# Kernel tuning notes

Measured on AMD Instinct MI355X. Metric: run time of the kernel, lower is better.

## Reference

```python
import jax, jax.numpy as jnp
import numpy as np

T = 16000        # signal length
N1 = 120         # first-order filters (J=12, Q=10)
NPSI2 = 14       # second-order filterbank size (Q2=1)
NPAIR = 553      # second-order coefficients -> 120 + 553 = 673 channels
SUB1 = 8         # subsample U1 before order 2
T2 = T // SUB1   # 2000
STR1 = 1000      # lowpass stride at length T  -> 16 output samples
STR2 = T2 // (T // STR1)  # 125 -> 16 output samples
LOG_EPS = 1e-6
BN_EPS = 1e-5


def _gauss_hat(N, xi, sigma):
    om = np.arange(N) / N
    return np.exp(-((om - xi) ** 2) / (2.0 * sigma ** 2)).astype(np.float32)


def _filterbank():
    Q = 10.0
    xi1 = 0.45 * 2.0 ** (-np.arange(N1) / Q)
    sig1 = np.maximum(xi1 * 0.1, 2.0 / T)
    psi1 = np.stack([_gauss_hat(T, x, s) for x, s in zip(xi1, sig1)])
    phi1 = _gauss_hat(T, 0.0, 0.4 / STR1)
    xi2 = 0.45 * 2.0 ** (-np.arange(NPSI2, dtype=np.float64))
    sig2 = np.maximum(xi2 * 0.2, 2.0 / T2)
    psi2 = np.stack([_gauss_hat(T2, x, s) for x, s in zip(xi2, sig2)])
    phi2 = _gauss_hat(T2, 0.0, 0.4 / STR2)
    pairs = [(i, j) for i in range(N1) for j in range(NPSI2) if xi2[j] < xi1[i] / 2.0]
    pairs = pairs[:NPAIR]
    assert len(pairs) == NPAIR
    pi1 = np.array([p[0] for p in pairs], np.int32)
    pi2 = np.array([p[1] for p in pairs], np.int32)
    return psi1, phi1, psi2, phi2, pi1, pi2


def setup_inputs():
    key = jax.random.key(0)
    ks = jax.random.split(key, 8)
    psi1, phi1, psi2, phi2, pi1, pi2 = _filterbank()
    B = 32
    inp = {
        "x": jax.random.normal(ks[0], (B, 1, T), jnp.float32),
        "psi1_hat": jnp.asarray(psi1),
        "phi1_hat": jnp.asarray(phi1),
        "psi2_hat": jnp.asarray(psi2),
        "phi2_hat": jnp.asarray(phi2),
        "gamma": jnp.ones((673,), jnp.float32),
        "beta": jnp.zeros((673,), jnp.float32),
        "W1": jax.random.normal(ks[1], (300, 673), jnp.float32) * 0.04,
        "b1": jnp.zeros((300,), jnp.float32),
        "W2": jax.random.normal(ks[2], (90, 300), jnp.float32) * 0.06,
        "b2": jnp.zeros((90,), jnp.float32),
        "W3": jax.random.normal(ks[3], (35, 90), jnp.float32) * 0.1,
        "b3": jnp.zeros((35,), jnp.float32),
        "pair_i1": jnp.asarray(pi1),
        "pair_i2": jnp.asarray(pi2),
    }
    return inp


def reference(x, psi1_hat, phi1_hat, psi2_hat, phi2_hat, gamma, beta,
              W1, b1, W2, b2, W3, b3, pair_i1, pair_i2):
    xs = x.squeeze(1)                                       # [B, T]
    Xf = jnp.fft.fft(xs)                                    # [B, T] c64
    # --- order 1: wavelet conv (freq-domain), modulus ---
    U1 = jnp.abs(jnp.fft.ifft(Xf[:, None, :] * psi1_hat[None]))        # [B, N1, T]
    # S1 = lowpass(U1) subsampled to 16 samples
    S1 = jnp.real(jnp.fft.ifft(jnp.fft.fft(U1) * phi1_hat))[..., ::STR1]  # [B, N1, 16]
    # --- order 2 on subsampled U1 ---
    U1sf = jnp.fft.fft(U1[..., ::SUB1])                     # [B, N1, T2]
    U2 = jnp.abs(jnp.fft.ifft(U1sf[:, pair_i1, :] * psi2_hat[pair_i2]))  # [B, NPAIR, T2]
    S2 = jnp.real(jnp.fft.ifft(jnp.fft.fft(U2) * phi2_hat))[..., ::STR2]  # [B, NPAIR, 16]
    S = jnp.concatenate([S1, S2], axis=1)                   # [B, 673, 16]
    # log-abs + temporal mean pooling
    f = jnp.mean(jnp.log(jnp.abs(S) + LOG_EPS), axis=-1)    # [B, 673]
    # BatchNorm1d (training mode: batch statistics)
    mu = jnp.mean(f, axis=0)
    var = jnp.var(f, axis=0)
    f = (f - mu) / jnp.sqrt(var + BN_EPS) * gamma + beta
    # MLP head
    h = jax.nn.relu(f @ W1.T + b1)
    h = jax.nn.relu(h @ W2.T + b2)
    return jax.nn.log_softmax(h @ W3.T + b3, axis=-1)
```

## Files before the change

kernel.cpp:

```cpp
#include <hip/hip_runtime.h>
#include <math.h>

typedef float2 cf;

__device__ __forceinline__ cf cadd(cf a, cf b){ return make_float2(a.x+b.x, a.y+b.y); }
__device__ __forceinline__ cf csub(cf a, cf b){ return make_float2(a.x-b.x, a.y-b.y); }
__device__ __forceinline__ cf cmul(cf a, cf b){ return make_float2(a.x*b.x - a.y*b.y, a.x*b.y + a.y*b.x); }

__device__ __forceinline__ int SW(int i){ return i ^ ((i>>4)&15); }
#define AT(x) s[SW(x)]
#define WFENCE asm volatile("" ::: "memory")

__device__ __forceinline__ int idivf(int a, int b){ return (a >= 0) ? a/b : -((-a + b - 1)/b); }
__device__ __forceinline__ int idivc(int a, int b){ return (a >= 0) ? (a + b - 1)/b : -((-a)/b); }

__device__ __forceinline__ int devB(int i){
  int jm = i/10 + 2;
  double kc = 900.0*exp2((double)(-jm));
  double sg = fmax(180.0*exp2((double)(-jm)), 2.0);
  return min(2000, (int)ceil(kc + 6.5*sg) + 1);
}

template<int N, int L, bool INV>
__device__ __forceinline__ void stage_r2(cf* __restrict__ s, const cf* __restrict__ tw, int tid, int nt){
  constexpr int Ls = L/2, nbf = N/2, tws = 16000/L;
  for (int q = tid; q < nbf; q += nt){
    int blk = q / Ls, j = q - blk*Ls;
    int base = blk*L + j;
    cf w1 = tw[tws*j]; if (INV) w1.y = -w1.y;
    if (!INV){
      cf a = AT(base), b = AT(base+Ls);
      AT(base) = cadd(a,b);
      AT(base+Ls) = cmul(csub(a,b), w1);
    } else {
      cf a = AT(base), b = cmul(AT(base+Ls), w1);
      AT(base) = cadd(a,b);
      AT(base+Ls) = csub(a,b);
    }
  }
}

template<int N, int L, bool INV>
__device__ __forceinline__ void stage_r4(cf* __restrict__ s, const cf* __restrict__ tw, int tid, int nt){
  constexpr int Ls = L/4, nbf = N/4, tws = 16000/L;
  for (int q = tid; q < nbf; q += nt){
    int blk = q / Ls, j = q - blk*Ls;
    int base = blk*L + j;
    cf w1 = tw[tws*j]; if (INV) w1.y = -w1.y;
    cf w2 = cmul(w1,w1), w3 = cmul(w2,w1);
    if (!INV){
      cf y0=AT(base), y1=AT(base+Ls), y2=AT(base+2*Ls), y3=AT(base+3*Ls);
      cf t0=cadd(y0,y2), t1=csub(y0,y2), t2=cadd(y1,y3), t3=csub(y1,y3);
      AT(base)      = cadd(t0,t2);
      AT(base+Ls)   = cmul(make_float2(t1.x + t3.y, t1.y - t3.x), w1);
      AT(base+2*Ls) = cmul(csub(t0,t2), w2);
      AT(base+3*Ls) = cmul(make_float2(t1.x - t3.y, t1.y + t3.x), w3);
    } else {
      cf z0=AT(base);
      cf z1=cmul(AT(base+Ls),   w1);
      cf z2=cmul(AT(base+2*Ls), w2);
      cf z3=cmul(AT(base+3*Ls), w3);
      cf t0=cadd(z0,z2), t1=csub(z0,z2), t2=cadd(z1,z3), t3=csub(z1,z3);
      AT(base)      = cadd(t0,t2);
      AT(base+Ls)   = make_float2(t1.x - t3.y, t1.y + t3.x);
      AT(base+2*Ls) = csub(t0,t2);
      AT(base+3*Ls) = make_float2(t1.x + t3.y, t1.y - t3.x);
    }
  }
}

template<int N, int L, bool INV>
__device__ __forceinline__ void stage_r5(cf* __restrict__ s, const cf* __restrict__ tw, int tid, int nt){
  constexpr int Ls = L/5, nbf = N/5, tws = 16000/L;
  const float C1 = 0.30901699437494742f, S1c = 0.95105651629515357f;
  const float C2 = -0.80901699437494745f, S2c = 0.58778525229247314f;
  for (int q = tid; q < nbf; q += nt){
    int blk = q / Ls, j = q - blk*Ls;
    int base = blk*L + j;
    cf w1 = tw[tws*j]; if (INV) w1.y = -w1.y;
    cf w2 = cmul(w1,w1), w3 = cmul(w2,w1), w4 = cmul(w2,w2);
    if (!INV){
      cf y0=AT(base), y1=AT(base+Ls), y2=AT(base+2*Ls), y3=AT(base+3*Ls), y4=AT(base+4*Ls);
      cf t1=cadd(y1,y4), t2=csub(y1,y4), t3=cadd(y2,y3), t4=csub(y2,y3);
      cf z0 = cadd(y0, cadd(t1,t3));
      cf m1 = make_float2(y0.x + C1*t1.x + C2*t3.x, y0.y + C1*t1.y + C2*t3.y);
      cf m2 = make_float2(y0.x + C2*t1.x + C1*t3.x, y0.y + C2*t1.y + C1*t3.y);
      cf wa = make_float2(S1c*t2.x + S2c*t4.x, S1c*t2.y + S2c*t4.y);
      cf wb = make_float2(S2c*t2.x - S1c*t4.x, S2c*t2.y - S1c*t4.y);
      cf o1 = make_float2(m1.x + wa.y, m1.y - wa.x);
      cf o4 = make_float2(m1.x - wa.y, m1.y + wa.x);
      cf o2 = make_float2(m2.x + wb.y, m2.y - wb.x);
      cf o3 = make_float2(m2.x - wb.y, m2.y + wb.x);
      AT(base) = z0;
      AT(base+Ls)   = cmul(o1,w1);
      AT(base+2*Ls) = cmul(o2,w2);
      AT(base+3*Ls) = cmul(o3,w3);
      AT(base+4*Ls) = cmul(o4,w4);
    } else {
      cf z0=AT(base);
      cf z1=cmul(AT(base+Ls),   w1);
      cf z2=cmul(AT(base+2*Ls), w2);
      cf z3=cmul(AT(base+3*Ls), w3);
      cf z4=cmul(AT(base+4*Ls), w4);
      cf t1=cadd(z1,z4), t2=csub(z1,z4), t3=cadd(z2,z3), t4=csub(z2,z3);
      cf y0 = cadd(z0, cadd(t1,t3));
      cf m1 = make_float2(z0.x + C1*t1.x + C2*t3.x, z0.y + C1*t1.y + C2*t3.y);
      cf m2 = make_float2(z0.x + C2*t1.x + C1*t3.x, z0.y + C2*t1.y + C1*t3.y);
      cf wa = make_float2(S1c*t2.x + S2c*t4.x, S1c*t2.y + S2c*t4.y);
      cf wb = make_float2(S2c*t2.x - S1c*t4.x, S2c*t2.y - S1c*t4.y);
      AT(base)      = y0;
      AT(base+Ls)   = make_float2(m1.x - wa.y, m1.y + wa.x);
      AT(base+2*Ls) = make_float2(m2.x - wb.y, m2.y + wb.x);
      AT(base+3*Ls) = make_float2(m2.x + wb.y, m2.y - wb.x);
      AT(base+4*Ls) = make_float2(m1.x + wa.y, m1.y - wa.x);
    }
  }
}

template<bool INV>
__device__ void fft16000(cf* s, const cf* tw, int tid, int nt){
  if (!INV){
    stage_r5<16000,16000,false>(s,tw,tid,nt); __syncthreads();
    stage_r5<16000, 3200,false>(s,tw,tid,nt); __syncthreads();
    stage_r5<16000,  640,false>(s,tw,tid,nt); __syncthreads();
    stage_r4<16000,  128,false>(s,tw,tid,nt); __syncthreads();
    stage_r4<16000,   32,false>(s,tw,tid,nt); __syncthreads();
    stage_r4<16000,    8,false>(s,tw,tid,nt); __syncthreads();
    stage_r2<16000,    2,false>(s,tw,tid,nt); __syncthreads();
  } else {
    stage_r2<16000,    2,true >(s,tw,tid,nt); __syncthreads();
    stage_r4<16000,    8,true >(s,tw,tid,nt); __syncthreads();
    stage_r4<16000,   32,true >(s,tw,tid,nt); __syncthreads();
    stage_r4<16000,  128,true >(s,tw,tid,nt); __syncthreads();
    stage_r5<16000,  640,true >(s,tw,tid,nt); __syncthreads();
    stage_r5<16000, 3200,true >(s,tw,tid,nt); __syncthreads();
    stage_r5<16000,16000,true >(s,tw,tid,nt); __syncthreads();
  }
}

template<bool INV>
__device__ void fft2000(cf* s, const cf* tw, int tid, int nt){
  if (!INV){
    stage_r5<2000,2000,false>(s,tw,tid,nt); __syncthreads();
    stage_r5<2000, 400,false>(s,tw,tid,nt); __syncthreads();
    stage_r5<2000,  80,false>(s,tw,tid,nt); __syncthreads();
    stage_r4<2000,  16,false>(s,tw,tid,nt); __syncthreads();
    stage_r4<2000,   4,false>(s,tw,tid,nt); __syncthreads();
  } else {
    stage_r4<2000,   4,true >(s,tw,tid,nt); __syncthreads();
    stage_r4<2000,  16,true >(s,tw,tid,nt); __syncthreads();
    stage_r5<2000,  80,true >(s,tw,tid,nt); __syncthreads();
    stage_r5<2000, 400,true >(s,tw,tid,nt); __syncthreads();
    stage_r5<2000,2000,true >(s,tw,tid,nt); __syncthreads();
  }
}

__device__ void fft8000i(cf* s, const cf* tw, int tid, int nt){
  stage_r4<8000,   4,true>(s,tw,tid,nt); __syncthreads();
  stage_r4<8000,  16,true>(s,tw,tid,nt); __syncthreads();
  stage_r4<8000,  64,true>(s,tw,tid,nt); __syncthreads();
  stage_r5<8000, 320,true>(s,tw,tid,nt); __syncthreads();
  stage_r5<8000,1600,true>(s,tw,tid,nt); __syncthreads();
  stage_r5<8000,8000,true>(s,tw,tid,nt); __syncthreads();
}
__device__ void fft4000i(cf* s, const cf* tw, int tid, int nt){
  stage_r2<4000,   2,true>(s,tw,tid,nt); __syncthreads();
  stage_r4<4000,   8,true>(s,tw,tid,nt); __syncthreads();
  stage_r4<4000,  32,true>(s,tw,tid,nt); __syncthreads();
  stage_r5<4000, 160,true>(s,tw,tid,nt); __syncthreads();
  stage_r5<4000, 800,true>(s,tw,tid,nt); __syncthreads();
  stage_r5<4000,4000,true>(s,tw,tid,nt); __syncthreads();
}
__device__ void fft1000i(cf* s, const cf* tw, int tid, int nt){
  stage_r2<1000,   2,true>(s,tw,tid,nt); __syncthreads();
  stage_r4<1000,   8,true>(s,tw,tid,nt); __syncthreads();
  stage_r5<1000,  40,true>(s,tw,tid,nt); __syncthreads();
  stage_r5<1000, 200,true>(s,tw,tid,nt); __syncthreads();
  stage_r5<1000,1000,true>(s,tw,tid,nt); __syncthreads();
}
__device__ void fft1000f(cf* s, const cf* tw, int tid, int nt){
  stage_r5<1000,1000,false>(s,tw,tid,nt); __syncthreads();
  stage_r5<1000, 200,false>(s,tw,tid,nt); __syncthreads();
  stage_r5<1000,  40,false>(s,tw,tid,nt); __syncthreads();
  stage_r4<1000,   8,false>(s,tw,tid,nt); __syncthreads();
  stage_r2<1000,   2,false>(s,tw,tid,nt); __syncthreads();
}
__device__ void fft500i(cf* s, const cf* tw, int tid, int nt){
  stage_r4<500,  4,true>(s,tw,tid,nt); __syncthreads();
  stage_r5<500, 20,true>(s,tw,tid,nt); __syncthreads();
  stage_r5<500,100,true>(s,tw,tid,nt); __syncthreads();
  stage_r5<500,500,true>(s,tw,tid,nt); __syncthreads();
}

__device__ __forceinline__ void fft250w(cf* s, const cf* tw, int lane){
  stage_r2<250,  2,true>(s,tw,lane,64); WFENCE;
  stage_r5<250, 10,true>(s,tw,lane,64); WFENCE;
  stage_r5<250, 50,true>(s,tw,lane,64); WFENCE;
  stage_r5<250,250,true>(s,tw,lane,64); WFENCE;
}
template<int M, bool INV>
__device__ __forceinline__ void fft_w(cf* s, const cf* tw, int lane){
  if constexpr (M==500){
    if constexpr (!INV){
      stage_r5<500,500,false>(s,tw,lane,64); WFENCE;
      stage_r5<500,100,false>(s,tw,lane,64); WFENCE;
      stage_r5<500, 20,false>(s,tw,lane,64); WFENCE;
      stage_r4<500,  4,false>(s,tw,lane,64); WFENCE;
    } else {
      stage_r4<500,  4,true>(s,tw,lane,64); WFENCE;
      stage_r5<500, 20,true>(s,tw,lane,64); WFENCE;
      stage_r5<500,100,true>(s,tw,lane,64); WFENCE;
      stage_r5<500,500,true>(s,tw,lane,64); WFENCE;
    }
  } else if constexpr (M==250){
    if constexpr (!INV){
      stage_r5<250,250,false>(s,tw,lane,64); WFENCE;
      stage_r5<250, 50,false>(s,tw,lane,64); WFENCE;
      stage_r5<250, 10,false>(s,tw,lane,64); WFENCE;
      stage_r2<250,  2,false>(s,tw,lane,64); WFENCE;
    } else {
      fft250w(s,tw,lane);
    }
  } else if constexpr (M==200){
    if constexpr (!INV){
      stage_r5<200,200,false>(s,tw,lane,64); WFENCE;
      stage_r5<200, 40,false>(s,tw,lane,64); WFENCE;
      stage_r4<200,  8,false>(s,tw,lane,64); WFENCE;
      stage_r2<200,  2,false>(s,tw,lane,64); WFENCE;
    } else {
      stage_r2<200,  2,true>(s,tw,lane,64); WFENCE;
      stage_r4<200,  8,true>(s,tw,lane,64); WFENCE;
      stage_r5<200, 40,true>(s,tw,lane,64); WFENCE;
      stage_r5<200,200,true>(s,tw,lane,64); WFENCE;
    }
  } else {
    if constexpr (!INV){
      stage_r5<125,125,false>(s,tw,lane,64); WFENCE;
      stage_r5<125, 25,false>(s,tw,lane,64); WFENCE;
      stage_r5<125,  5,false>(s,tw,lane,64); WFENCE;
    } else {
      stage_r5<125,  5,true>(s,tw,lane,64); WFENCE;
      stage_r5<125, 25,true>(s,tw,lane,64); WFENCE;
      stage_r5<125,125,true>(s,tw,lane,64); WFENCE;
    }
  }
}

__device__ __forceinline__ int pos16000(int k){
  int k0=k%5; k/=5; int k1=k%5; k/=5; int k2=k%5; k/=5;
  int k3=k&3; k>>=2; int k4=k&3; k>>=2; int k5=k&3; k>>=2;
  return k0*3200 + k1*640 + k2*128 + k3*32 + k4*8 + k5*2 + k;
}
__device__ __forceinline__ int pos8000(int k){
  int k0=k%5; k/=5; int k1=k%5; k/=5; int k2=k%5; k/=5;
  int k3=k&3, k4=(k>>2)&3, k5=k>>4;
  return k0*1600 + k1*320 + k2*64 + k3*16 + k4*4 + k5;
}
__device__ __forceinline__ int pos4000(int k){
  int k0=k%5; k/=5; int k1=k%5; k/=5; int k2=k%5; k/=5;
  int k3=k&3, k4=(k>>2)&3, k5=k>>4;
  return k0*800 + k1*160 + k2*32 + k3*8 + k4*2 + k5;
}
__device__ __forceinline__ int pos2000(int k){
  int k0=k%5; k/=5; int k1=k%5; k/=5; int k2=k%5; k/=5;
  int k3=k&3, k4=k>>2;
  return k0*400 + k1*80 + k2*16 + k3*4 + k4;
}
__device__ __forceinline__ int pos1000(int k){
  int k0=k%5; k/=5; int k1=k%5; k/=5; int k2=k%5; k/=5;
  int k3=k&3, k4=k>>2;
  return k0*200 + k1*40 + k2*8 + k3*2 + k4;
}
__device__ __forceinline__ int pos500(int k){
  int k0=k%5; k/=5; int k1=k%5; k/=5; int k2=k%5; k/=5;
  return k0*100 + k1*20 + k2*4 + k;
}
__device__ __forceinline__ int pos250(int k){
  int k0=k%5; k/=5; int k1=k%5; k/=5; int k2=k%5; k/=5;
  return k0*50 + k1*10 + k2*2 + k;
}
__device__ __forceinline__ int pos200(int k){
  int k0=k%5; k/=5; int k1=k%5; k/=5;
  int k2=k&3, k3=k>>2;
  return k0*40 + k1*8 + k2*2 + k3;
}
__device__ __forceinline__ int pos125(int k){
  int k0=k%5; k/=5; int k1=k%5; k/=5;
  return k0*25 + k1*5 + k;
}

template<int M> __device__ __forceinline__ int posM(int k){
  if constexpr (M==16000) return pos16000(k);
  else if constexpr (M==8000) return pos8000(k);
  else if constexpr (M==4000) return pos4000(k);
  else return pos2000(k);
}
template<int M> __device__ __forceinline__ int posS(int k){
  if constexpr (M==500) return pos500(k);
  else if constexpr (M==250) return pos250(k);
  else if constexpr (M==200) return pos200(k);
  else return pos125(k);
}
template<int M> __device__ __forceinline__ void fftM_inv(cf* s, const cf* tw, int tid, int nt){
  if constexpr (M==16000) fft16000<true>(s,tw,tid,nt);
  else if constexpr (M==8000) fft8000i(s,tw,tid,nt);
  else if constexpr (M==4000) fft4000i(s,tw,tid,nt);
  else fft2000<true>(s,tw,tid,nt);
}


__global__ void k_tw(cf* __restrict__ tw){
  int j = blockIdx.x*blockDim.x + threadIdx.x;
  if (j < 16000){
    double a = -6.283185307179586476925286766559 * (double)j / 16000.0;
    tw[j] = make_float2((float)cos(a), (float)sin(a));
  }
}

__global__ void k_btab(const float* __restrict__ phi1, const float* __restrict__ phi2,
                       float* __restrict__ h1g, float* __restrict__ h2g){
  int i = blockIdx.x*blockDim.x + threadIdx.x;
  const double TWO_PI = 6.283185307179586476925286766559;
  if (i < 5201){
    int d = i - 2600;
    double a = 0.0;
    for (int k = 0; k < 64; ++k) a += (double)phi1[k]*cos(TWO_PI*(double)(k*d)/16000.0);
    h1g[i] = (float)(a/16000.0 - (double)phi1[0]/32000.0);
  } else if (i == 5201){
    h1g[5201] = phi1[0]*(1.f/32000.f);
  } else if (i < 5202 + 661){
    int j = i - 5202; int d = j - 330;
    double a = 0.0;
    for (int k = 0; k < 64; ++k) a += (double)phi2[k]*cos(TWO_PI*(double)(k*d)/2000.0);
    h2g[j] = (float)(a/2000.0 - (double)phi2[0]/4000.0);
  } else if (i == 5202 + 661){
    h2g[661] = phi2[0]*(1.f/4000.f);
  }
}

__global__ __launch_bounds__(1024) void k_classify(const int* __restrict__ pi2,
                                                   int* __restrict__ list5, int* __restrict__ list4){
  __shared__ int w5[16], w4[16];
  int p = threadIdx.x;
  for (int t = p; t < 493; t += 1024) list5[t] = 0;
  for (int t = p; t < 60;  t += 1024) list4[t] = 0;
  bool valid = p < 553;
  int j2 = valid ? pi2[p] : 99;
  bool f5 = valid && (j2 >= 5);
  bool f4 = valid && (j2 < 5);
  unsigned long long m5 = __ballot(f5);
  unsigned long long m4 = __ballot(f4);
  int lane = p & 63, wid = p >> 6;
  if (lane == 0){ w5[wid] = __popcll(m5); w4[wid] = __popcll(m4); }
  __syncthreads();
  if (valid){
    int b5 = 0, b4 = 0;
    for (int w = 0; w < wid; ++w){ b5 += w5[w]; b4 += w4[w]; }
    unsigned long long lm = (1ull << lane) - 1ull;
    if (f5) list5[b5 + __popcll(m5 & lm)] = p;
    if (f4) list4[b4 + __popcll(m4 & lm)] = p;
  }
}

__global__ __launch_bounds__(1024) void k_fftx(const float* __restrict__ x, cf* __restrict__ Xf,
                                               const cf* __restrict__ tw){
  extern __shared__ cf s[];
  int b = blockIdx.x;
  int tid = threadIdx.x, nt = blockDim.x;
  for (int n = tid; n < 16000; n += nt) AT(n) = make_float2(x[b*16000 + n], 0.f);
  __syncthreads();
  fft16000<false>(s, tw, tid, nt);
  for (int k = tid; k < 16000; k += nt) Xf[b*16000 + k] = AT(pos16000(k));
}

template<int M, int ST, int NF, int I0, int NT>
__global__ __launch_bounds__(NT) void kf(const cf* __restrict__ Xf, const float* __restrict__ psi1,
                                         const float* __restrict__ h1g, const cf* __restrict__ tw,
                                         cf* __restrict__ U1sf, float* __restrict__ S1){
  extern __shared__ cf s[];
  constexpr int NW = NT/64;
  int b = blockIdx.x / NF;
  int i = I0 + (blockIdx.x - b*NF);
  int tid = threadIdx.x, wid = tid>>6, lane = tid&63;
  double x1 = 0.45 * exp2((double)(-i) / 10.0);
  double kc = 16000.0 * x1;
  double sg = fmax(1600.0 * x1, 2.0);
  int k0 = max(0, (int)floor(kc - 6.5*sg));
  int k1 = min(16000, (int)ceil(kc + 6.5*sg) + 1);
  int W = k1 - k0;
  for (int n = tid; n < M; n += NT) s[n] = make_float2(0.f, 0.f);
  __syncthreads();
  const cf* X = Xf + (size_t)b*16000 + k0;
  const float* P = psi1 + (size_t)i*16000 + k0;
  for (int j = tid; j < W; j += NT){
    cf v = X[j]; float pf = P[j];
    int pp = posM<M>(j);
    AT(pp) = make_float2(v.x*pf, v.y*pf);
  }
  __syncthreads();
  fftM_inv<M>(s, tw, tid, NT);
  constexpr int R = (M + NT - 1)/NT;
  float mreg[R]; float tsum = 0.f;
  const float inv = 1.f/16000.f;
  #pragma unroll
  for (int r = 0; r < R; ++r){
    int n = tid + r*NT;
    if (n < M){ cf v = AT(n); mreg[r] = sqrtf(v.x*v.x + v.y*v.y)*inv; tsum += mreg[r]; }
    else mreg[r] = 0.f;
  }
  float* fl = (float*)s;
  float* part = (float*)(s + M);
  __syncthreads();
  #pragma unroll
  for (int r = 0; r < R; ++r){ int n = tid + r*NT; if (n < M) fl[n] = mreg[r]; }
  #pragma unroll
  for (int o = 32; o > 0; o >>= 1) tsum += __shfl_xor(tsum, o);
  if (lane == 0) part[wid] = tsum;
  __syncthreads();
  if (tid == 0){ float tt = 0.f; for (int w = 0; w < NW; ++w) tt += part[w]; part[NW] = tt; }
  __syncthreads();
  float stot = part[NW];
  float c1 = h1g[5201];
  for (int t = wid; t < 16; t += NW){
    int mlo = (1000*t - 2600)/ST;
    int mhi = (1000*t + 2600)/ST;
    float acc = 0.f;
    for (int m = mlo + lane; m <= mhi; m += 64){
      int mm = m; if (mm < 0) mm += M; else if (mm >= M) mm -= M;
      acc = fmaf(fl[mm], h1g[1000*t - m*ST + 2600], acc);
    }
    #pragma unroll
    for (int o = 32; o > 0; o >>= 1) acc += __shfl_xor(acc, o);
    if (lane == 0) S1[((size_t)b*120 + i)*16 + t] = (float)ST*(acc + c1*stot);
  }
  constexpr int K = 8/ST;
  float d0 = fl[tid*K];
  float d1 = 0.f;
  { int m2 = tid + 1024; if (m2 < 2000) d1 = fl[m2*K]; }
  __syncthreads();
  AT(tid) = make_float2(d0, 0.f);
  { int m2 = tid + 1024; if (m2 < 2000) AT(m2) = make_float2(d1, 0.f); }
  __syncthreads();
  fft2000<false>(s, tw, tid, NT);
  int B = devB(i);
  cf* out = U1sf + ((size_t)b*120 + i)*2000;
  for (int k = tid; k < B; k += NT) out[k] = AT(pos2000(k));
}

template<int M, int ST, int NF, int I0>
__global__ __launch_bounds__(256) void k_nb(const cf* __restrict__ Xf, const float* __restrict__ psi1,
                                            const float* __restrict__ h1g, const cf* __restrict__ tw,
                                            cf* __restrict__ U1sf, float* __restrict__ S1){
  extern __shared__ cf s[];
  float* fl = (float*)(s + M);
  float* part = fl + M;
  int b = blockIdx.x / NF;
  int i = I0 + (blockIdx.x - b*NF);
  int tid = threadIdx.x, wid = tid>>6, lane = tid&63;
  double x1 = 0.45 * exp2((double)(-i)/10.0);
  double kc = 16000.0*x1, sg = fmax(1600.0*x1, 2.0);
  int k0 = max(0,(int)floor(kc-6.5*sg));
  int k1 = min(16000,(int)ceil(kc+6.5*sg)+1);
  int W = k1-k0;
  for (int n = tid; n < M; n += 256) s[n] = make_float2(0.f,0.f);
  __syncthreads();
  const cf* X = Xf + (size_t)b*16000 + k0;
  const float* P = psi1 + (size_t)i*16000 + k0;
  for (int j = tid; j < W; j += 256){
    cf v = X[j]; float pf = P[j];
    int pp = (M==2000) ? pos2000(j) : pos1000(j);
    AT(pp) = make_float2(v.x*pf, v.y*pf);
  }
  __syncthreads();
  if constexpr (M==2000) fft2000<true>(s,tw,tid,256); else fft1000i(s,tw,tid,256);
  float tsum = 0.f;
  for (int n = tid; n < M; n += 256){
    cf v = AT(n);
    float mg = sqrtf(v.x*v.x+v.y*v.y)*(1.f/16000.f);
    fl[n] = mg; tsum += mg;
  }
  #pragma unroll
  for (int o=32;o>0;o>>=1) tsum += __shfl_xor(tsum,o);
  if (lane==0) part[wid] = tsum;
  __syncthreads();
  float stot = part[0]+part[1]+part[2]+part[3];
  float c1 = h1g[5201];
  float* S1o = S1 + ((size_t)b*120+i)*16;
  for (int r = 0; r < 4; ++r){
    int t = wid + 4*r;
    int mlo = idivc(1000*t-2600,ST), mhi = idivf(1000*t+2600,ST);
    float acc = 0.f;
    for (int m = mlo+lane; m <= mhi; m += 64){
      int mm = m; if (mm<0) mm+=M; else if (mm>=M) mm-=M;
      acc = fmaf(fl[mm], h1g[1000*t - m*ST + 2600], acc);
    }
    #pragma unroll
    for (int o=32;o>0;o>>=1) acc += __shfl_xor(acc,o);
    if (lane==0) S1o[t] = (float)ST*(acc + c1*stot);
  }
  __syncthreads();
  for (int n = tid; n < M; n += 256) AT(n) = make_float2(fl[n], 0.f);
  __syncthreads();
  if constexpr (M==2000) fft2000<false>(s,tw,tid,256); else fft1000f(s,tw,tid,256);
  int B = devB(i);
  const float sc = 2000.f/(float)M;
  cf* out = U1sf + ((size_t)b*120+i)*2000;
  for (int k = tid; k < B; k += 256){
    cf v = AT((M==2000)?pos2000(k):pos1000(k));
    out[k] = make_float2(v.x*sc, v.y*sc);
  }
}

template<int M, int SPAD, int ST, int NF, int I0, int WPB>
__global__ __launch_bounds__(WPB*64) void k_nw(const cf* __restrict__ Xf, const float* __restrict__ psi1,
                                               const float* __restrict__ h1g, const cf* __restrict__ tw,
                                               cf* __restrict__ U1sf, float* __restrict__ S1){
  extern __shared__ cf sh[];
  int wid = threadIdx.x >> 6, lane = threadIdx.x & 63;
  int q = blockIdx.x*WPB + wid;
  int filt = q >> 5, b = q & 31;
  int i = I0 + filt;
  cf* s = sh + wid*SPAD;
  float* fl = ((float*)(sh + WPB*SPAD)) + wid*SPAD;
  double x1 = 0.45 * exp2((double)(-i)/10.0);
  double kc = 16000.0*x1, sg = fmax(1600.0*x1, 2.0);
  int k0 = max(0,(int)floor(kc-6.5*sg));
  int k1 = min(16000,(int)ceil(kc+6.5*sg)+1);
  int W = k1-k0;
  for (int n = lane; n < SPAD; n += 64) s[n] = make_float2(0.f,0.f);
  WFENCE;
  const cf* X = Xf + (size_t)b*16000 + k0;
  const float* P = psi1 + (size_t)i*16000 + k0;
  for (int j = lane; j < W; j += 64){
    cf v = X[j]; float pf = P[j];
    AT(posS<M>(j)) = make_float2(v.x*pf, v.y*pf);
  }
  WFENCE;
  fft_w<M,true>(s,tw,lane);
  float tsum = 0.f;
  for (int n = lane; n < M; n += 64){
    cf v = AT(n);
    float mg = sqrtf(v.x*v.x+v.y*v.y)*(1.f/16000.f);
    fl[n] = mg; tsum += mg;
  }
  WFENCE;
  #pragma unroll
  for (int o=32;o>0;o>>=1) tsum += __shfl_xor(tsum,o);
  float c1 = h1g[5201];
  float* S1o = S1 + ((size_t)b*120+i)*16;
  for (int t = 0; t < 16; ++t){
    int mlo = idivc(1000*t-2600,ST), mhi = idivf(1000*t+2600,ST);
    float acc = 0.f;
    for (int m = mlo+lane; m <= mhi; m += 64){
      int mm = m; if (mm<0) mm+=M; else if (mm>=M) mm-=M;
      acc = fmaf(fl[mm], h1g[1000*t - m*ST + 2600], acc);
    }
    #pragma unroll
    for (int o=32;o>0;o>>=1) acc += __shfl_xor(acc,o);
    if (lane==0) S1o[t] = (float)ST*(acc + c1*tsum);
  }
  for (int n = lane; n < M; n += 64) AT(n) = make_float2(fl[n], 0.f);
  WFENCE;
  fft_w<M,false>(s,tw,lane);
  int B = devB(i);
  const float sc = 2000.f/(float)M;
  cf* out = U1sf + ((size_t)b*120+i)*2000;
  for (int k = lane; k < B; k += 64){
    cf v = AT(posS<M>(k));
    out[k] = make_float2(v.x*sc, v.y*sc);
  }
}

__global__ __launch_bounds__(256) void k_sec5(const cf* __restrict__ U1sf, const float* __restrict__ psi2,
                                              const float* __restrict__ h2g, const cf* __restrict__ tw,
                                              const int* __restrict__ pi1, const int* __restrict__ pi2,
                                              const int* __restrict__ list5, float* __restrict__ S2){
  __shared__ cf sall[4*256];
  __shared__ float flall[4*256];
  int wid = threadIdx.x >> 6, lane = threadIdx.x & 63;
  int q = blockIdx.x*4 + wid;
  int p = list5[q >> 5];
  int b = q & 31;
  int i1 = pi1[p], j2 = pi2[p];
  cf* s = sall + wid*256;
  float* fl2 = flall + wid*256;
  double xc = exp2((double)(-j2));
  double kc = 900.0*xc, sg = fmax(180.0*xc, 2.0);
  int k0 = max(0, (int)floor(kc - 6.5*sg));
  int k1 = min(2000, (int)ceil(kc + 6.5*sg) + 1);
  int W = k1 - k0;
  for (int n = lane; n < 256; n += 64) s[n] = make_float2(0.f, 0.f);
  WFENCE;
  const cf* U = U1sf + (size_t)(b*120 + i1)*2000 + k0;
  const float* F = psi2 + j2*2000 + k0;
  for (int j = lane; j < W; j += 64){
    cf v = U[j]; float f = F[j];
    AT(pos250(j)) = make_float2(v.x*f, v.y*f);
  }
  WFENCE;
  fft250w(s, tw, lane);
  float tsum = 0.f;
  #pragma unroll
  for (int r = 0; r < 4; ++r){
    int n = lane + r*64;
    if (n < 250){
      cf v = AT(n);
      float mg = sqrtf(v.x*v.x + v.y*v.y)*(1.f/2000.f);
      fl2[n] = mg; tsum += mg;
    }
  }
  WFENCE;
  #pragma unroll
  for (int o = 32; o > 0; o >>= 1) tsum += __shfl_xor(tsum, o);
  float stot = tsum;
  float c2 = h2g[661];
  float* S2o = S2 + (size_t)(b*553 + p)*16;
  for (int t = 0; t < 16; ++t){
    int mlo = (125*t - 330 + 7) >> 3;
    int mhi = (125*t + 330) >> 3;
    float acc = 0.f;
    for (int m = mlo + lane; m <= mhi; m += 64){
      int mm = m; if (mm < 0) mm += 250; else if (mm >= 250) mm -= 250;
      acc = fmaf(fl2[mm], h2g[125*t - m*8 + 330], acc);
    }
    #pragma unroll
    for (int o = 32; o > 0; o >>= 1) acc += __shfl_xor(acc, o);
    if (lane == 0) S2o[t] = 8.f*(acc + c2*stot);
  }
}

__global__ __launch_bounds__(128) void k_secbig(const cf* __restrict__ U1sf, const float* __restrict__ psi2,
                                                const float* __restrict__ h2g, const cf* __restrict__ tw,
                                                const int* __restrict__ pi1, const int* __restrict__ pi2,
                                                const int* __restrict__ list4, float* __restrict__ S2){
  extern __shared__ cf s[];
  float* fl2 = (float*)(s + 2000);
  float* part = fl2 + 2000;
  int p = list4[blockIdx.x >> 5];
  int b = blockIdx.x & 31;
  int tid = threadIdx.x, wid = tid>>6, lane = tid&63;
  int i1 = pi1[p], j2 = pi2[p];
  int M2, s2l;
  if (j2 == 4){ M2 = 500;  s2l = 2; }
  else if (j2 == 3){ M2 = 1000; s2l = 1; }
  else { M2 = 2000; s2l = 0; }
  int ST2 = 1 << s2l;
  double xc = exp2((double)(-j2));
  double kc = 900.0*xc, sg = fmax(180.0*xc, 2.0);
  int k0 = max(0, (int)floor(kc - 6.5*sg));
  int k1 = min(2000, (int)ceil(kc + 6.5*sg) + 1);
  int W = k1 - k0;
// ... 105 lines not shown
                                              float* __restrict__ out){
  __shared__ float lg[35];
  int b = blockIdx.x;
  int tid = threadIdx.x, wid = tid >> 6, lane = tid & 63;
  for (int r = wid; r < 35; r += 4){
    float acc = 0.f;
    for (int k = lane; k < 90; k += 64) acc = fmaf(h2[b*90 + k], W3[r*90 + k], acc);
    #pragma unroll
    for (int o = 32; o > 0; o >>= 1) acc += __shfl_down(acc, o);
    if (lane == 0) lg[r] = acc + b3[r];
  }
  __syncthreads();
  if (tid < 64){
    float v = (tid < 35) ? lg[tid] : -1e30f;
    float mx = v;
    #pragma unroll
    for (int o = 32; o > 0; o >>= 1) mx = fmaxf(mx, __shfl_xor(mx, o));
    float e = (tid < 35) ? expf(v - mx) : 0.f;
    float se = e;
    #pragma unroll
    for (int o = 32; o > 0; o >>= 1) se += __shfl_xor(se, o);
    if (tid < 35) out[b*35 + tid] = v - mx - logf(se);
  }
}


extern "C" void kernel_launch(void* const* d_in, const int* in_sizes, int n_in,
                              void* d_out, int out_size, void* d_ws, size_t ws_size,
                              hipStream_t stream){
  const float* x     = (const float*)d_in[0];
  const float* psi1  = (const float*)d_in[1];
  const float* phi1  = (const float*)d_in[2];
  const float* psi2  = (const float*)d_in[3];
  const float* phi2  = (const float*)d_in[4];
  const float* gamma = (const float*)d_in[5];
  const float* beta  = (const float*)d_in[6];
  const float* W1    = (const float*)d_in[7];
  const float* b1    = (const float*)d_in[8];
  const float* W2    = (const float*)d_in[9];
  const float* b2    = (const float*)d_in[10];
  const float* W3    = (const float*)d_in[11];
  const float* b3    = (const float*)d_in[12];
  const int*   pi1   = (const int*)d_in[13];
  const int*   pi2   = (const int*)d_in[14];

  char* ws = (char*)d_ws;
  constexpr size_t o_tw = 0;
  constexpr size_t o_Xf = o_tw + (size_t)16000*sizeof(cf);
  constexpr size_t o_U  = o_Xf + (size_t)32*16000*sizeof(cf);
  constexpr size_t o_S1 = o_U  + (size_t)3840*2000*sizeof(cf);
  constexpr size_t o_S2 = o_S1 + (size_t)3840*16*sizeof(float);
  constexpr size_t o_l5 = o_S2 + (size_t)17696*16*sizeof(float);
  constexpr size_t o_l4 = o_l5 + (size_t)512*sizeof(int);
  constexpr size_t o_fn = o_l4 + (size_t)64*sizeof(int);
  constexpr size_t o_h1 = o_fn + (size_t)32*673*sizeof(float);
  constexpr size_t o_h2 = o_h1 + (size_t)5202*sizeof(float);
  constexpr size_t o_m1 = o_h2 + (size_t)662*sizeof(float);
  constexpr size_t o_m2 = o_m1 + (size_t)32*300*sizeof(float);

  cf*    tw    = (cf*)(ws + o_tw);
  cf*    Xf    = (cf*)(ws + o_Xf);
  cf*    U1sf  = (cf*)(ws + o_U);
  float* S1b   = (float*)(ws + o_S1);
  float* S2b   = (float*)(ws + o_S2);
  int*   list5 = (int*)(ws + o_l5);
  int*   list4 = (int*)(ws + o_l4);
  float* fnbuf = (float*)(ws + o_fn);
  float* h1g   = (float*)(ws + o_h1);
  float* h2g   = (float*)(ws + o_h2);
  float* m1buf = (float*)(ws + o_m1);
  float* m2buf = (float*)(ws + o_m2);

  hipFuncSetAttribute((const void*)k_fftx, hipFuncAttributeMaxDynamicSharedMemorySize, 131072);
  hipFuncSetAttribute((const void*)kf<16000,1,13, 0,1024>, hipFuncAttributeMaxDynamicSharedMemorySize, 131072);
  hipFuncSetAttribute((const void*)kf< 8000,2,10,13,1024>, hipFuncAttributeMaxDynamicSharedMemorySize, 131072);

  k_tw<<<63, 256, 0, stream>>>(tw);
  k_btab<<<23, 256, 0, stream>>>(phi1, phi2, h1g, h2g);
  k_classify<<<1, 1024, 0, stream>>>(pi2, list5, list4);
  k_fftx<<<32, 1024, 128000, stream>>>(x, Xf, tw);
  kf<16000,1,13, 0,1024><<<32*13, 1024, 16000*8 + 17*4, stream>>>(Xf, psi1, h1g, tw, U1sf, S1b);
  kf< 8000,2,10,13,1024><<<32*10, 1024,  8000*8 + 17*4, stream>>>(Xf, psi1, h1g, tw, U1sf, S1b);
  kf< 4000,4,10,23,1024><<<32*10, 1024,  4000*8 + 17*4, stream>>>(Xf, psi1, h1g, tw, U1sf, S1b);
  k_nb<2000, 8,10,33><<<32*10, 256, 2000*8 + 2000*4 + 5*4, stream>>>(Xf, psi1, h1g, tw, U1sf, S1b);
  k_nb<1000,16,10,43><<<32*10, 256, 1000*8 + 1000*4 + 5*4, stream>>>(Xf, psi1, h1g, tw, U1sf, S1b);
  k_nw< 500,512, 32,10,53,4><<< 80, 256, 4*512*12, stream>>>(Xf, psi1, h1g, tw, U1sf, S1b);
  k_nw< 250,256, 64,10,63,8><<< 40, 512, 8*256*12, stream>>>(Xf, psi1, h1g, tw, U1sf, S1b);
  k_nw< 200,208, 80,10,73,8><<< 40, 512, 8*208*12, stream>>>(Xf, psi1, h1g, tw, U1sf, S1b);
  k_nw< 125,128,128,37,83,8><<<148, 512, 8*128*12, stream>>>(Xf, psi1, h1g, tw, U1sf, S1b);
  k_sec5<<<(493*32)/4, 256, 0, stream>>>(U1sf, psi2, h2g, tw, pi1, pi2, list5, S2b);
  k_secbig<<<60*32, 128, 2000*8 + 2000*4 + 4*4, stream>>>(U1sf, psi2, h2g, tw, pi1, pi2, list4, S2b);
  k_fbn<<<673, 64, 0, stream>>>(S1b, S2b, gamma, beta, fnbuf);
  k_mlp1<<<1200, 512, 0, stream>>>(fnbuf, W1, b1, m1buf);
  k_mlp2<<<360, 512, 0, stream>>>(m1buf, W2, b2, m2buf);
  k_mlp3<<<32, 256, 0, stream>>>(m2buf, W3, b3, (float*)d_out);
}
```

Before: 392.4 us.

## Compute order-1 lowpass in frequency domain and resize narrowband FFT lengths

For filters 33 and up, the order-1 lowpass S1 is no longer a spatial-domain convolution over U1 with an h1g table. It is now a 64-bin frequency-domain evaluation using phi1 and twiddles, taken after the forward FFT that is already needed for U1sf. The per-band FFT sizes change to lengths that are multiples of 16 (1600, 640, 320, 160 instead of 1000, 500, 250, 125), so the 16-point output grid aligns with the subsampling. This also removes the separate float magnitude buffer. The aim is to cut the scalar convolution loops and shared-memory use, at the cost of somewhat larger FFTs and a possible accuracy change from truncating to 64 frequency bins.

Measured after the change: 366.6 us. 1.07x faster.

```diff
diff --git a/kernel.cpp b/kernel.cpp
--- a/kernel.cpp
+++ b/kernel.cpp
@@ -11,8 +11,9 @@
 #define AT(x) s[SW(x)]
 #define WFENCE asm volatile("" ::: "memory")
 
-__device__ __forceinline__ int idivf(int a, int b){ return (a >= 0) ? a/b : -((-a + b - 1)/b); }
-__device__ __forceinline__ int idivc(int a, int b){ return (a >= 0) ? (a + b - 1)/b : -((-a)/b); }
+template<bool WAVE> __device__ __forceinline__ void SYf(){
+  if constexpr (WAVE) { WFENCE; } else __syncthreads();
+}
 
 __device__ __forceinline__ int devB(int i){
   int jm = i/10 + 2;
@@ -178,70 +179,98 @@
   stage_r5<1000, 200,true>(s,tw,tid,nt); __syncthreads();
   stage_r5<1000,1000,true>(s,tw,tid,nt); __syncthreads();
 }
-__device__ void fft1000f(cf* s, const cf* tw, int tid, int nt){
-  stage_r5<1000,1000,false>(s,tw,tid,nt); __syncthreads();
-  stage_r5<1000, 200,false>(s,tw,tid,nt); __syncthreads();
-  stage_r5<1000,  40,false>(s,tw,tid,nt); __syncthreads();
-  stage_r4<1000,   8,false>(s,tw,tid,nt); __syncthreads();
-  stage_r2<1000,   2,false>(s,tw,tid,nt); __syncthreads();
-}
 __device__ void fft500i(cf* s, const cf* tw, int tid, int nt){
   stage_r4<500,  4,true>(s,tw,tid,nt); __syncthreads();
   stage_r5<500, 20,true>(s,tw,tid,nt); __syncthreads();
   stage_r5<500,100,true>(s,tw,tid,nt); __syncthreads();
   stage_r5<500,500,true>(s,tw,tid,nt); __syncthreads();
 }
-
 __device__ __forceinline__ void fft250w(cf* s, const cf* tw, int lane){
   stage_r2<250,  2,true>(s,tw,lane,64); WFENCE;
   stage_r5<250, 10,true>(s,tw,lane,64); WFENCE;
   stage_r5<250, 50,true>(s,tw,lane,64); WFENCE;
   stage_r5<250,250,true>(s,tw,lane,64); WFENCE;
 }
-template<int M, bool INV>
-__device__ __forceinline__ void fft_w(cf* s, const cf* tw, int lane){
-  if constexpr (M==500){
-    if constexpr (!INV){
-      stage_r5<500,500,false>(s,tw,lane,64); WFENCE;
-      stage_r5<500,100,false>(s,tw,lane,64); WFENCE;
-      stage_r5<500, 20,false>(s,tw,lane,64); WFENCE;
-      stage_r4<500,  4,false>(s,tw,lane,64); WFENCE;
+
+template<int M, bool INV, bool WAVE>
+__device__ __forceinline__ void fftg(cf* s, const cf* tw, int tid, int nt){
+  if constexpr (M==2000){
+    if constexpr (INV){
+      stage_r4<2000,4,true>(s,tw,tid,nt); SYf<WAVE>();
+      stage_r4<2000,16,true>(s,tw,tid,nt); SYf<WAVE>();
+      stage_r5<2000,80,true>(s,tw,tid,nt); SYf<WAVE>();
+      stage_r5<2000,400,true>(s,tw,tid,nt); SYf<WAVE>();
+      stage_r5<2000,2000,true>(s,tw,tid,nt); SYf<WAVE>();
     } else {
-      stage_r4<500,  4,true>(s,tw,lane,64); WFENCE;
-      stage_r5<500, 20,true>(s,tw,lane,64); WFENCE;
-      stage_r5<500,100,true>(s,tw,lane,64); WFENCE;
-      stage_r5<500,500,true>(s,tw,lane,64); WFENCE;
-    }
-  } else if constexpr (M==250){
-    if constexpr (!INV){
-      stage_r5<250,250,false>(s,tw,lane,64); WFENCE;
-      stage_r5<250, 50,false>(s,tw,lane,64); WFENCE;
-      stage_r5<250, 10,false>(s,tw,lane,64); WFENCE;
-      stage_r2<250,  2,false>(s,tw,lane,64); WFENCE;
+      stage_r5<2000,2000,false>(s,tw,tid,nt); SYf<WAVE>();
+      stage_r5<2000,400,false>(s,tw,tid,nt); SYf<WAVE>();
+      stage_r5<2000,80,false>(s,tw,tid,nt); SYf<WAVE>();
+      stage_r4<2000,16,false>(s,tw,tid,nt); SYf<WAVE>();
+      stage_r4<2000,4,false>(s,tw,tid,nt); SYf<WAVE>();
+    }
+  } else if constexpr (M==1600){
+    if constexpr (INV){
+      stage_r4<1600,4,true>(s,tw,tid,nt); SYf<WAVE>();
+      stage_r4<1600,16,true>(s,tw,tid,nt); SYf<WAVE>();
+      stage_r4<1600,64,true>(s,tw,tid,nt); SYf<WAVE>();
+      stage_r5<1600,320,true>(s,tw,tid,nt); SYf<WAVE>();
+      stage_r5<1600,1600,true>(s,tw,tid,nt); SYf<WAVE>();
     } else {
-      fft250w(s,tw,lane);
+      stage_r5<1600,1600,false>(s,tw,tid,nt); SYf<WAVE>();
+      stage_r5<1600,320,false>(s,tw,tid,nt); SYf<WAVE>();
+      stage_r4<1600,64,false>(s,tw,tid,nt); SYf<WAVE>();
+      stage_r4<1600,16,false>(s,tw,tid,nt); SYf<WAVE>();
+      stage_r4<1600,4,false>(s,tw,tid,nt); SYf<WAVE>();
+    }
+  } else if constexpr (M==640){
+    if constexpr (INV){
+      stage_r2<640,2,true>(s,tw,tid,nt); SYf<WAVE>();
+      stage_r4<640,8,true>(s,tw,tid,nt); SYf<WAVE>();
+      stage_r4<640,32,true>(s,tw,tid,nt); SYf<WAVE>();
+      stage_r4<640,128,true>(s,tw,tid,nt); SYf<WAVE>();
+      stage_r5<640,640,true>(s,tw,tid,nt); SYf<WAVE>();
+    } else {
+      stage_r5<640,640,false>(s,tw,tid,nt); SYf<WAVE>();
+      stage_r4<640,128,false>(s,tw,tid,nt); SYf<WAVE>();
+      stage_r4<640,32,false>(s,tw,tid,nt); SYf<WAVE>();
+      stage_r4<640,8,false>(s,tw,tid,nt); SYf<WAVE>();
+      stage_r2<640,2,false>(s,tw,tid,nt); SYf<WAVE>();
+    }
+  } else if constexpr (M==320){
+    if constexpr (INV){
+      stage_r4<320,4,true>(s,tw,tid,nt); SYf<WAVE>();
+      stage_r4<320,16,true>(s,tw,tid,nt); SYf<WAVE>();
+      stage_r4<320,64,true>(s,tw,tid,nt); SYf<WAVE>();
+      stage_r5<320,320,true>(s,tw,tid,nt); SYf<WAVE>();
+    } else {
+      stage_r5<320,320,false>(s,tw,tid,nt); SYf<WAVE>();
+      stage_r4<320,64,false>(s,tw,tid,nt); SYf<WAVE>();
+      stage_r4<320,16,false>(s,tw,tid,nt); SYf<WAVE>();
+      stage_r4<320,4,false>(s,tw,tid,nt); SYf<WAVE>();
     }
   } else if constexpr (M==200){
-    if constexpr (!INV){
-      stage_r5<200,200,false>(s,tw,lane,64); WFENCE;
-      stage_r5<200, 40,false>(s,tw,lane,64); WFENCE;
-      stage_r4<200,  8,false>(s,tw,lane,64); WFENCE;
-      stage_r2<200,  2,false>(s,tw,lane,64); WFENCE;
+    if constexpr (INV){
+      stage_r2<200,2,true>(s,tw,tid,nt); SYf<WAVE>();
+      stage_r4<200,8,true>(s,tw,tid,nt); SYf<WAVE>();
+      stage_r5<200,40,true>(s,tw,tid,nt); SYf<WAVE>();
+      stage_r5<200,200,true>(s,tw,tid,nt); SYf<WAVE>();
     } else {
-      stage_r2<200,  2,true>(s,tw,lane,64); WFENCE;
-      stage_r4<200,  8,true>(s,tw,lane,64); WFENCE;
-      stage_r5<200, 40,true>(s,tw,lane,64); WFENCE;
-      stage_r5<200,200,true>(s,tw,lane,64); WFENCE;
+      stage_r5<200,200,false>(s,tw,tid,nt); SYf<WAVE>();
+      stage_r5<200,40,false>(s,tw,tid,nt); SYf<WAVE>();
+      stage_r4<200,8,false>(s,tw,tid,nt); SYf<WAVE>();
+      stage_r2<200,2,false>(s,tw,tid,nt); SYf<WAVE>();
     }
   } else {
-    if constexpr (!INV){
-      stage_r5<125,125,false>(s,tw,lane,64); WFENCE;
-      stage_r5<125, 25,false>(s,tw,lane,64); WFENCE;
-      stage_r5<125,  5,false>(s,tw,lane,64); WFENCE;
+    if constexpr (INV){
+      stage_r2<160,2,true>(s,tw,tid,nt); SYf<WAVE>();
+      stage_r4<160,8,true>(s,tw,tid,nt); SYf<WAVE>();
+      stage_r4<160,32,true>(s,tw,tid,nt); SYf<WAVE>();
+      stage_r5<160,160,true>(s,tw,tid,nt); SYf<WAVE>();
     } else {
-      stage_r5<125,  5,true>(s,tw,lane,64); WFENCE;
-      stage_r5<125, 25,true>(s,tw,lane,64); WFENCE;
-      stage_r5<125,125,true>(s,tw,lane,64); WFENCE;
+      stage_r5<160,160,false>(s,tw,tid,nt); SYf<WAVE>();
+      stage_r4<160,32,false>(s,tw,tid,nt); SYf<WAVE>();
+      stage_r4<160,8,false>(s,tw,tid,nt); SYf<WAVE>();
+      stage_r2<160,2,false>(s,tw,tid,nt); SYf<WAVE>();
     }
   }
 }
@@ -266,14 +295,29 @@
   int k3=k&3, k4=k>>2;
   return k0*400 + k1*80 + k2*16 + k3*4 + k4;
 }
+__device__ __forceinline__ int pos1600(int k){
+  int k0=k%5; k/=5; int k1=k%5; k/=5;
+  int k2=k&3; k>>=2; int k3=k&3; k>>=2;
+  return k0*320 + k1*64 + k2*16 + k3*4 + k;
+}
 __device__ __forceinline__ int pos1000(int k){
   int k0=k%5; k/=5; int k1=k%5; k/=5; int k2=k%5; k/=5;
   int k3=k&3, k4=k>>2;
   return k0*200 + k1*40 + k2*8 + k3*2 + k4;
 }
+__device__ __forceinline__ int pos640(int k){
+  int k0=k%5; k/=5;
+  int k1=k&3; k>>=2; int k2=k&3; k>>=2; int k3=k&3; k>>=2;
+  return k0*128 + k1*32 + k2*8 + k3*2 + k;
+}
 __device__ __forceinline__ int pos500(int k){
   int k0=k%5; k/=5; int k1=k%5; k/=5; int k2=k%5; k/=5;
   return k0*100 + k1*20 + k2*4 + k;
+}
+__device__ __forceinline__ int pos320(int k){
+  int k0=k%5; k/=5;
+  int k1=k&3; k>>=2; int k2=k&3; k>>=2;
+  return k0*64 + k1*16 + k2*4 + k;
 }
 __device__ __forceinline__ int pos250(int k){
   int k0=k%5; k/=5; int k1=k%5; k/=5; int k2=k%5; k/=5;
@@ -284,9 +328,10 @@
   int k2=k&3, k3=k>>2;
   return k0*40 + k1*8 + k2*2 + k3;
 }
-__device__ __forceinline__ int pos125(int k){
-  int k0=k%5; k/=5; int k1=k%5; k/=5;
-  return k0*25 + k1*5 + k;
+__device__ __forceinline__ int pos160(int k){
+  int k0=k%5; k/=5;
+  int k1=k&3; k>>=2; int k2=k&3; k>>=2;
+  return k0*32 + k1*8 + k2*2 + k;
 }
 
 template<int M> __device__ __forceinline__ int posM(int k){
@@ -295,11 +340,13 @@
   else if constexpr (M==4000) return pos4000(k);
   else return pos2000(k);
 }
-template<int M> __device__ __forceinline__ int posS(int k){
-  if constexpr (M==500) return pos500(k);
-  else if constexpr (M==250) return pos250(k);
+template<int M> __device__ __forceinline__ int posN(int k){
+  if constexpr (M==2000) return pos2000(k);
+  else if constexpr (M==1600) return pos1600(k);
+  else if constexpr (M==640) return pos640(k);
+  else if constexpr (M==320) return pos320(k);
   else if constexpr (M==200) return pos200(k);
-  else return pos125(k);
+  else return pos160(k);
 }
 template<int M> __device__ __forceinline__ void fftM_inv(cf* s, const cf* tw, int tid, int nt){
   if constexpr (M==16000) fft16000<true>(s,tw,tid,nt);
@@ -447,13 +494,11 @@
   for (int k = tid; k < B; k += NT) out[k] = AT(pos2000(k));
 }
 
-template<int M, int ST, int NF, int I0>
-__global__ __launch_bounds__(256) void k_nb(const cf* __restrict__ Xf, const float* __restrict__ psi1,
-                                            const float* __restrict__ h1g, const cf* __restrict__ tw,
+template<int M, int NF, int I0>
+__global__ __launch_bounds__(256) void k_n2(const cf* __restrict__ Xf, const float* __restrict__ psi1,
+                                            const float* __restrict__ phi1, const cf* __restrict__ tw,
                                             cf* __restrict__ U1sf, float* __restrict__ S1){
   extern __shared__ cf s[];
-  float* fl = (float*)(s + M);
-  float* part = fl + M;
   int b = blockIdx.x / NF;
   int i = I0 + (blockIdx.x - b*NF);
   int tid = threadIdx.x, wid = tid>>6, lane = tid&63;
@@ -468,60 +513,50 @@
   const float* P = psi1 + (size_t)i*16000 + k0;
   for (int j = tid; j < W; j += 256){
     cf v = X[j]; float pf = P[j];
-    int pp = (M==2000) ? pos2000(j) : pos1000(j);
-    AT(pp) = make_float2(v.x*pf, v.y*pf);
-  }
-  __syncthreads();
-  if constexpr (M==2000) fft2000<true>(s,tw,tid,256); else fft1000i(s,tw,tid,256);
-  float tsum = 0.f;
+    AT(posN<M>(j)) = make_float2(v.x*pf, v.y*pf);
+  }
+  __syncthreads();
+  fftg<M,true,false>(s,tw,tid,256);
   for (int n = tid; n < M; n += 256){
     cf v = AT(n);
-    float mg = sqrtf(v.x*v.x+v.y*v.y)*(1.f/16000.f);
-    fl[n] = mg; tsum += mg;
-  }
-  #pragma unroll
-  for (int o=32;o>0;o>>=1) tsum += __shfl_xor(tsum,o);
-  if (lane==0) part[wid] = tsum;
-  __syncthreads();
-  float stot = part[0]+part[1]+part[2]+part[3];
-  float c1 = h1g[5201];
-  float* S1o = S1 + ((size_t)b*120+i)*16;
-  for (int r = 0; r < 4; ++r){
-    int t = wid + 4*r;
-    int mlo = idivc(1000*t-2600,ST), mhi = idivf(1000*t+2600,ST);
-    float acc = 0.f;
-    for (int m = mlo+lane; m <= mhi; m += 64){
-      int mm = m; if (mm<0) mm+=M; else if (mm>=M) mm-=M;
-      acc = fmaf(fl[mm], h1g[1000*t - m*ST + 2600], acc);
-    }
-    #pragma unroll
-    for (int o=32;o>0;o>>=1) acc += __shfl_xor(acc,o);
-    if (lane==0) S1o[t] = (float)ST*(acc + c1*stot);
-  }
-  __syncthreads();
-  for (int n = tid; n < M; n += 256) AT(n) = make_float2(fl[n], 0.f);
-  __syncthreads();
-  if constexpr (M==2000) fft2000<false>(s,tw,tid,256); else fft1000f(s,tw,tid,256);
+    AT(n) = make_float2(sqrtf(v.x*v.x+v.y*v.y)*(1.f/16000.f), 0.f);
+  }
+  __syncthreads();
+  fftg<M,false,false>(s,tw,tid,256);
+  {
+    int k = lane;
+    cf g = AT(posN<M>(k));
+    float ph = phi1[k];
+    float gx = g.x*ph, gy = g.y*ph;
+    float* S1o = S1 + ((size_t)b*120+i)*16;
+    for (int r = 0; r < 4; ++r){
+      int t = wid + 4*r;
+      cf e = tw[1000*((k*t)&15)];
+      float val = gx*e.x + gy*e.y;
+      #pragma unroll
+      for (int o = 32; o > 0; o >>= 1) val += __shfl_xor(val, o);
+      if (lane == 0) S1o[t] = val*(1.f/(float)M);
+    }
+  }
   int B = devB(i);
   const float sc = 2000.f/(float)M;
   cf* out = U1sf + ((size_t)b*120+i)*2000;
   for (int k = tid; k < B; k += 256){
-    cf v = AT((M==2000)?pos2000(k):pos1000(k));
+    cf v = AT(posN<M>(k));
     out[k] = make_float2(v.x*sc, v.y*sc);
   }
 }
 
-template<int M, int SPAD, int ST, int NF, int I0, int WPB>
-__global__ __launch_bounds__(WPB*64) void k_nw(const cf* __restrict__ Xf, const float* __restrict__ psi1,
-                                               const float* __restrict__ h1g, const cf* __restrict__ tw,
-                                               cf* __restrict__ U1sf, float* __restrict__ S1){
+template<int M, int SPAD, int NF, int I0, int WPB>
+__global__ __launch_bounds__(WPB*64) void k_nw2(const cf* __restrict__ Xf, const float* __restrict__ psi1,
+                                                const float* __restrict__ phi1, const cf* __restrict__ tw,
+                                                cf* __restrict__ U1sf, float* __restrict__ S1){
   extern __shared__ cf sh[];
   int wid = threadIdx.x >> 6, lane = threadIdx.x & 63;
   int q = blockIdx.x*WPB + wid;
   int filt = q >> 5, b = q & 31;
   int i = I0 + filt;
   cf* s = sh + wid*SPAD;
-  float* fl = ((float*)(sh + WPB*SPAD)) + wid*SPAD;
   double x1 = 0.45 * exp2((double)(-i)/10.0);
   double kc = 16000.0*x1, sg = fmax(1600.0*x1, 2.0);
   int k0 = max(0,(int)floor(kc-6.5*sg));
@@ -533,40 +568,35 @@
   const float* P = psi1 + (size_t)i*16000 + k0;
   for (int j = lane; j < W; j += 64){
     cf v = X[j]; float pf = P[j];
-    AT(posS<M>(j)) = make_float2(v.x*pf, v.y*pf);
+    AT(posN<M>(j)) = make_float2(v.x*pf, v.y*pf);
   }
   WFENCE;
-  fft_w<M,true>(s,tw,lane);
-  float tsum = 0.f;
+  fftg<M,true,true>(s,tw,lane,64);
   for (int n = lane; n < M; n += 64){
     cf v = AT(n);
-    float mg = sqrtf(v.x*v.x+v.y*v.y)*(1.f/16000.f);
-    fl[n] = mg; tsum += mg;
+    AT(n) = make_float2(sqrtf(v.x*v.x+v.y*v.y)*(1.f/16000.f), 0.f);
   }
   WFENCE;
-  #pragma unroll
-  for (int o=32;o>0;o>>=1) tsum += __shfl_xor(tsum,o);
-  float c1 = h1g[5201];
-  float* S1o = S1 + ((size_t)b*120+i)*16;
-  for (int t = 0; t < 16; ++t){
-    int mlo = idivc(1000*t-2600,ST), mhi = idivf(1000*t+2600,ST);
-    float acc = 0.f;
-    for (int m = mlo+lane; m <= mhi; m += 64){
-      int mm = m; if (mm<0) mm+=M; else if (mm>=M) mm-=M;
-      acc = fmaf(fl[mm], h1g[1000*t - m*ST + 2600], acc);
-    }
-    #pragma unroll
-    for (int o=32;o>0;o>>=1) acc += __shfl_xor(acc,o);
-    if (lane==0) S1o[t] = (float)ST*(acc + c1*tsum);
-  }
-  for (int n = lane; n < M; n += 64) AT(n) = make_float2(fl[n], 0.f);
-  WFENCE;
-  fft_w<M,false>(s,tw,lane);
+  fftg<M,false,true>(s,tw,lane,64);
+  {
+    int k = lane;
+    cf g = AT(posN<M>(k));
+    float ph = phi1[k];
+    float gx = g.x*ph, gy = g.y*ph;
+    float* S1o = S1 + ((size_t)b*120+i)*16;
+    for (int t = 0; t < 16; ++t){
+      cf e = tw[1000*((k*t)&15)];
+      float val = gx*e.x + gy*e.y;
+      #pragma unroll
+      for (int o = 32; o > 0; o >>= 1) val += __shfl_xor(val, o);
+      if (lane == 0) S1o[t] = val*(1.f/(float)M);
+    }
+  }
   int B = devB(i);
   const float sc = 2000.f/(float)M;
   cf* out = U1sf + ((size_t)b*120+i)*2000;
   for (int k = lane; k < B; k += 64){
-    cf v = AT(posS<M>(k));
+    cf v = AT(posN<M>(k));
     out[k] = make_float2(v.x*sc, v.y*sc);
   }
 }
@@ -838,12 +868,12 @@
   kf<16000,1,13, 0,1024><<<32*13, 1024, 16000*8 + 17*4, stream>>>(Xf, psi1, h1g, tw, U1sf, S1b);
   kf< 8000,2,10,13,1024><<<32*10, 1024,  8000*8 + 17*4, stream>>>(Xf, psi1, h1g, tw, U1sf, S1b);
   kf< 4000,4,10,23,1024><<<32*10, 1024,  4000*8 + 17*4, stream>>>(Xf, psi1, h1g, tw, U1sf, S1b);
-  k_nb<2000, 8,10,33><<<32*10, 256, 2000*8 + 2000*4 + 5*4, stream>>>(Xf, psi1, h1g, tw, U1sf, S1b);
-  k_nb<1000,16,10,43><<<32*10, 256, 1000*8 + 1000*4 + 5*4, stream>>>(Xf, psi1, h1g, tw, U1sf, S1b);
-  k_nw< 500,512, 32,10,53,4><<< 80, 256, 4*512*12, stream>>>(Xf, psi1, h1g, tw, U1sf, S1b);
-  k_nw< 250,256, 64,10,63,8><<< 40, 512, 8*256*12, stream>>>(Xf, psi1, h1g, tw, U1sf, S1b);
-  k_nw< 200,208, 80,10,73,8><<< 40, 512, 8*208*12, stream>>>(Xf, psi1, h1g, tw, U1sf, S1b);
-  k_nw< 125,128,128,37,83,8><<<148, 512, 8*128*12, stream>>>(Xf, psi1, h1g, tw, U1sf, S1b);
+  k_n2<2000,10,33><<<32*10, 256, 2000*8, stream>>>(Xf, psi1, phi1, tw, U1sf, S1b);
+  k_n2<1600,10,43><<<32*10, 256, 1600*8, stream>>>(Xf, psi1, phi1, tw, U1sf, S1b);
+  k_nw2<640,640,10,53,4><<< 80, 256, 4*640*8, stream>>>(Xf, psi1, phi1, tw, U1sf, S1b);
+  k_nw2<320,320,10,63,8><<< 40, 512, 8*320*8, stream>>>(Xf, psi1, phi1, tw, U1sf, S1b);
+  k_nw2<200,208,10,73,8><<< 40, 512, 8*208*8, stream>>>(Xf, psi1, phi1, tw, U1sf, S1b);
+  k_nw2<160,160,37,83,8><<<148, 512, 8*160*8, stream>>>(Xf, psi1, phi1, tw, U1sf, S1b);
   k_sec5<<<(493*32)/4, 256, 0, stream>>>(U1sf, psi2, h2g, tw, pi1, pi2, list5, S2b);
   k_secbig<<<60*32, 128, 2000*8 + 2000*4 + 4*4, stream>>>(U1sf, psi2, h2g, tw, pi1, pi2, list4, S2b);
   k_fbn<<<673, 64, 0, stream>>>(S1b, S2b, gamma, beta, fnbuf);
```
